# Kernel tuning notes

Measured on AMD Instinct MI355X. Metric: run time of the kernel, lower is better.

The kernel has to match this reference:

```python
import jax, jax.numpy as jnp
import numpy as np

NNZ = 3355443          # int(4096*4096*(1-0.8))
IN_FEATURES = 4096
OUT_FEATURES = 4096
BATCH = 64
ACTIVE_THRESHOLD = 0.01


def setup_inputs() -> dict:
    key = jax.random.key(0)
    k1, k2, k3, k4 = jax.random.split(key, 4)
    x = jax.random.uniform(k1, (BATCH, IN_FEATURES), dtype=jnp.float32)
    row_indices = jax.random.randint(k2, (NNZ,), 0, OUT_FEATURES, dtype=jnp.int32)
    col_indices = jax.random.randint(k3, (NNZ,), 0, IN_FEATURES, dtype=jnp.int32)
    values = jax.random.normal(k4, (NNZ,), dtype=jnp.float32)
    bias = jnp.zeros((OUT_FEATURES,), dtype=jnp.float32)
    return {"x": x, "row_indices": row_indices, "col_indices": col_indices,
            "values": values, "bias": bias}


def reference(x, row_indices, col_indices, values, bias):
    # Event-driven gating: only columns with x > threshold contribute.
    # Equivalent to masking x, then a standard COO spmv per batch row.
    xm = jnp.where(x > ACTIVE_THRESHOLD, x, jnp.zeros((), x.dtype))   # [B, in]
    contrib = values[None, :] * xm[:, col_indices]                    # [B, nnz]
    out = jnp.zeros((x.shape[0], bias.shape[0]), dtype=x.dtype)
    out = out.at[:, row_indices].add(contrib)                         # scatter-add over rows
    return out + bias[None, :]
```

## Files before the change

### kernel.cpp

```cpp
#include <hip/hip_runtime.h>
#include <hip/hip_bf16.h>
#include <stdint.h>

#define IN_F 4096
#define OUT_F 4096
#define NBKT 256
#define SBLOCKS 820
#define REC_PER_SB 4096
#define SMAX 14336u
#define THRESH 0.01f

typedef unsigned int u32;
typedef unsigned short u16;
typedef unsigned char u8;
typedef __attribute__((ext_vector_type(8))) short short8;
typedef __attribute__((ext_vector_type(4))) float f32x4;

static constexpr size_t pad256(size_t x) { return (x + 255u) & ~(size_t)255u; }
static constexpr size_t WS_XB   = 0;
static constexpr size_t WS_CUR  = pad256(WS_XB + (size_t)512 * 64 * 8 * 2);
static constexpr size_t WS_BINS = pad256(WS_CUR + (size_t)NBKT * 4);
static constexpr size_t WS_NEEDED = WS_BINS + (size_t)NBKT * SMAX * 4;

static __device__ __forceinline__ u16 f2bf(float v) {
  __hip_bfloat16 h = __float2bfloat16(v);
  return *reinterpret_cast<u16*>(&h);
}

__global__ __launch_bounds__(256) void k_init(u32* __restrict__ gcursor) {
  gcursor[threadIdx.x] = 0u;
}

__global__ __launch_bounds__(512) void k_scatter(const int* __restrict__ rows,
                                                 const int* __restrict__ cols,
                                                 const float* __restrict__ vals, u32 nnz,
                                                 const float* __restrict__ x,
                                                 u16* __restrict__ xB,
                                                 u32* __restrict__ gcursor,
                                                 u32* __restrict__ sortb) {
  __shared__ u32 cnt[NBKT];
  __shared__ u32 pref[NBKT + 1];
  __shared__ u32 gbase[NBKT];
  __shared__ u32 srt[REC_PER_SB];
  __shared__ u8 srtb[REC_PER_SB];
  const int tid = threadIdx.x;
  const int lane = tid & 63;
  const int wid = tid >> 6;

  if (blockIdx.x < 64) {
    const int g = blockIdx.x * 512 + tid;
    const int b = g & 63;
    const int kg = g >> 6;
    const float* src = x + (size_t)b * IN_F + kg * 8;
    const f32x4 a0 = *reinterpret_cast<const f32x4*>(src);
    const f32x4 a1 = *reinterpret_cast<const f32x4*>(src + 4);
    short8 o;
#pragma unroll
    for (int e = 0; e < 4; ++e) {
      float v = a0[e]; v = (v > THRESH) ? v : 0.0f; o[e] = (short)f2bf(v);
    }
#pragma unroll
    for (int e = 0; e < 4; ++e) {
      float v = a1[e]; v = (v > THRESH) ? v : 0.0f; o[4 + e] = (short)f2bf(v);
    }
    *reinterpret_cast<short8*>(xB + ((size_t)kg * 64 + b) * 8) = o;
  }

  if (tid < NBKT) cnt[tid] = 0;
  __syncthreads();
  const u32 base_i = blockIdx.x * (u32)REC_PER_SB;
  u32 rec[8], bkt[8], rk[8];
#pragma unroll
  for (int j = 0; j < 8; ++j) {
    const u32 i = base_i + (u32)j * 512u + tid;
    bkt[j] = 0xffffffffu;
    if (i < nnz) {
      const u32 r = (u32)rows[i] & 4095u;
      const u32 c = (u32)cols[i] & 4095u;
      rec[j] = (c << 20) | ((r & 15u) << 16) | (u32)f2bf(vals[i]);
      bkt[j] = r >> 4;
      rk[j] = atomicAdd(&cnt[bkt[j]], 1u);
    }
  }
  __syncthreads();
  if (wid == 0) {
    u32 a[4]; u32 s = 0;
#pragma unroll
    for (int j = 0; j < 4; ++j) { a[j] = cnt[lane * 4 + j]; s += a[j]; }
    u32 xx = s;
#pragma unroll
    for (int d = 1; d < 64; d <<= 1) {
      const u32 y = (u32)__shfl_up((int)xx, d, 64);
      if (lane >= d) xx += y;
    }
    u32 e = xx - s;
#pragma unroll
    for (int j = 0; j < 4; ++j) { pref[lane * 4 + j] = e; e += a[j]; }
    if (lane == 63) pref[256] = e;
  }
  __syncthreads();
#pragma unroll
  for (int j = 0; j < 8; ++j)
    if (bkt[j] != 0xffffffffu) {
      const u32 pos = pref[bkt[j]] + rk[j];
      srt[pos] = rec[j];
      srtb[pos] = (u8)bkt[j];
    }
  if (tid < NBKT) {
    const u32 len = pref[tid + 1] - pref[tid];
    gbase[tid] = len ? atomicAdd(&gcursor[tid], len) : 0u;
  }
  __syncthreads();
  const u32 tot = pref[NBKT];
#pragma unroll
  for (int j = 0; j < 8; ++j) {
    const u32 i = (u32)j * 512u + tid;
    if (i < tot) {
      const u32 t = srtb[i];
      const u32 off = gbase[t] + (i - pref[t]);
      if (off < SMAX) sortb[(size_t)t * SMAX + off] = srt[i];
    }
  }
}

__global__ __launch_bounds__(1024, 1) void k_accum(const u32* __restrict__ sortb,
                                                   const u32* __restrict__ ntot,
                                                   const u16* __restrict__ xB,
                                                   const float* __restrict__ bias,
                                                   float* __restrict__ out) {
  __shared__ float W[16 * 1024];
  const int tid = threadIdx.x;
  const int lane = tid & 63;
  const int w = tid >> 6;
  const u32 t = blockIdx.x;
  u32 n = ntot[t];
  if (n > SMAX) n = SMAX;
  const u32* bin = sortb + (size_t)t * SMAX;
  u32 rec[14];
#pragma unroll
  for (int j = 0; j < 14; ++j) {
    const u32 i = (u32)j * 1024u + tid;
    rec[j] = (i < n) ? bin[i] : 0u;
  }

  f32x4 acc0 = {0.f, 0.f, 0.f, 0.f}, acc1 = {0.f, 0.f, 0.f, 0.f};
  f32x4 acc2 = {0.f, 0.f, 0.f, 0.f}, acc3 = {0.f, 0.f, 0.f, 0.f};
  const int row = lane & 15;
  const int e8 = (lane >> 4) * 8;

  for (int q = 0; q < 4; ++q) {
    __syncthreads();
    const f32x4 z = {0.f, 0.f, 0.f, 0.f};
#pragma unroll
    for (int j = 0; j < 4; ++j)
      *reinterpret_cast<f32x4*>(&W[j * 4096 + tid * 4]) = z;
    __syncthreads();
#pragma unroll
    for (int j = 0; j < 14; ++j) {
      const u32 i = (u32)j * 1024u + tid;
      if (i < n) {
        const u32 rc = rec[j];
        if ((rc >> 30) == (u32)q) {
          const u32 rl = (rc >> 16) & 15u;
          const u32 cl = ((rc >> 20) & 1023u) ^ ((rl & 7u) << 3);
          unsafeAtomicAdd(&W[rl * 1024u + cl], __uint_as_float(rc << 16));
        }
      }
    }
    __syncthreads();
#pragma unroll
    for (int s = 0; s < 2; ++s) {
      const int klb = w * 64 + s * 32 + e8;
      const int sw = klb ^ ((row & 7) << 3);
      const f32x4 wa = *reinterpret_cast<const f32x4*>(&W[row * 1024 + sw]);
      const f32x4 wb = *reinterpret_cast<const f32x4*>(&W[row * 1024 + (sw + 4)]);
      short8 af;
#pragma unroll
      for (int e = 0; e < 4; ++e) af[e] = (short)f2bf(wa[e]);
#pragma unroll
      for (int e = 0; e < 4; ++e) af[4 + e] = (short)f2bf(wb[e]);
      const int kabs = q * 1024 + klb;
      const u16* bp = xB + (size_t)(kabs >> 3) * 512 + (u32)row * 8;
      const short8 b0 = *reinterpret_cast<const short8*>(bp);
      const short8 b1 = *reinterpret_cast<const short8*>(bp + 128);
      const short8 b2 = *reinterpret_cast<const short8*>(bp + 256);
      const short8 b3 = *reinterpret_cast<const short8*>(bp + 384);
      acc0 = __builtin_amdgcn_mfma_f32_16x16x32_bf16(af, b0, acc0, 0, 0, 0);
      acc1 = __builtin_amdgcn_mfma_f32_16x16x32_bf16(af, b1, acc1, 0, 0, 0);
      acc2 = __builtin_amdgcn_mfma_f32_16x16x32_bf16(af, b2, acc2, 0, 0, 0);
      acc3 = __builtin_amdgcn_mfma_f32_16x16x32_bf16(af, b3, acc3, 0, 0, 0);
    }
  }
  __syncthreads();
  {
    const int ccol = lane & 15;
    const int rb = (lane >> 4) * 4;
#pragma unroll
    for (int qq = 0; qq < 4; ++qq) W[((w * 4 + 0) * 16 + rb + qq) * 16 + ccol] = acc0[qq];
#pragma unroll
    for (int qq = 0; qq < 4; ++qq) W[((w * 4 + 1) * 16 + rb + qq) * 16 + ccol] = acc1[qq];
#pragma unroll
    for (int qq = 0; qq < 4; ++qq) W[((w * 4 + 2) * 16 + rb + qq) * 16 + ccol] = acc2[qq];
#pragma unroll
    for (int qq = 0; qq < 4; ++qq) W[((w * 4 + 3) * 16 + rb + qq) * 16 + ccol] = acc3[qq];
  }
  __syncthreads();
  const int rl = tid & 15;
  const int b = tid >> 4;
  float sum = bias[t * 16u + rl];
#pragma unroll
  for (int w2 = 0; w2 < 16; ++w2)
    sum += W[((w2 * 4 + (b >> 4)) * 16 + rl) * 16 + (b & 15)];
  out[(size_t)b * OUT_F + t * 16u + rl] = sum;
}

__global__ __launch_bounds__(256) void k_bias_init(const float* __restrict__ bias,
                                                   float* __restrict__ out) {
  const int i = blockIdx.x * 256 + threadIdx.x;
  if (i < 64 * OUT_F) out[i] = bias[i & (OUT_F - 1)];
}

__global__ __launch_bounds__(256) void k_fallback(const int* __restrict__ rows,
                                                  const int* __restrict__ cols,
                                                  const float* __restrict__ vals,
                                                  const float* __restrict__ x,
                                                  float* __restrict__ out, int nnz) {
  const int gw = (int)(((u32)blockIdx.x * blockDim.x + threadIdx.x) >> 6);
  const int lane = threadIdx.x & 63;
  const int nw = (int)(((u32)gridDim.x * blockDim.x) >> 6);
  for (int i = gw; i < nnz; i += nw) {
    const int r = rows[i];
    const int c = cols[i];
    const float v = vals[i];
    const float xv = x[lane * IN_F + c];
    if (xv > THRESH) atomicAdd(&out[(size_t)lane * OUT_F + r], v * xv);
  }
}

extern "C" void kernel_launch(void* const* d_in, const int* in_sizes, int n_in,
                              void* d_out, int out_size, void* d_ws, size_t ws_size,
                              hipStream_t stream) {
  const float* x = (const float*)d_in[0];
  const int* rows = (const int*)d_in[1];
  const int* cols = (const int*)d_in[2];
  const float* vals = (const float*)d_in[3];
  const float* bias = (const float*)d_in[4];
  float* out = (float*)d_out;
  const int nnz = in_sizes[1];

  if (ws_size >= WS_NEEDED && nnz <= SBLOCKS * REC_PER_SB) {
    u16* xB = (u16*)((char*)d_ws + WS_XB);
    u32* gcursor = (u32*)((char*)d_ws + WS_CUR);
    u32* sortb = (u32*)((char*)d_ws + WS_BINS);
    k_init<<<1, 256, 0, stream>>>(gcursor);
    k_scatter<<<SBLOCKS, 512, 0, stream>>>(rows, cols, vals, (u32)nnz, x, xB,
                                           gcursor, sortb);
    k_accum<<<NBKT, 1024, 0, stream>>>(sortb, gcursor, xB, bias, out);
  } else {
    k_bias_init<<<(64 * OUT_F + 255) / 256, 256, 0, stream>>>(bias, out);
    k_fallback<<<4096, 256, 0, stream>>>(rows, cols, vals, x, out, nnz);
  }
}
```

Measured before the change: 65.32 us.

## Fuse init, scatter and accumulate into one cooperative kernel with grid syncs

Replaces the three kernel launches (cursor init, bucket scatter, per-bucket accumulate) with a single cooperative kernel of 256 blocks of 1024 threads, separated by grid-wide barriers and using a shared-memory union for both phases. This removes two launch gaps and the extra pass over gcursor. In exchange the scatter phase now runs on 256 large blocks with about 13K records each instead of 820 smaller blocks, which lowers occupancy and parallelism for that phase. It also adds the cost of cooperative launch and grid syncs.

Result: slower. 120.4 us (+84.3%).

```diff
diff --git a/kernel.cpp b/kernel.cpp
--- a/kernel.cpp
+++ b/kernel.cpp
@@ -1,12 +1,13 @@
 #include <hip/hip_runtime.h>
 #include <hip/hip_bf16.h>
+#include <hip/hip_cooperative_groups.h>
 #include <stdint.h>
 
 #define IN_F 4096
 #define OUT_F 4096
 #define NBKT 256
-#define SBLOCKS 820
-#define REC_PER_SB 4096
+#define NBLK 256
+#define REC_PER_SB 13120
 #define SMAX 14336u
 #define THRESH 0.01f
 
@@ -16,6 +17,8 @@
 typedef __attribute__((ext_vector_type(8))) short short8;
 typedef __attribute__((ext_vector_type(4))) float f32x4;
 
+namespace cg = cooperative_groups;
+
 static constexpr size_t pad256(size_t x) { return (x + 255u) & ~(size_t)255u; }
 static constexpr size_t WS_XB   = 0;
 static constexpr size_t WS_CUR  = pad256(WS_XB + (size_t)512 * 64 * 8 * 2);
@@ -27,28 +30,37 @@
   return *reinterpret_cast<u16*>(&h);
 }
 
-__global__ __launch_bounds__(256) void k_init(u32* __restrict__ gcursor) {
-  gcursor[threadIdx.x] = 0u;
-}
-
-__global__ __launch_bounds__(512) void k_scatter(const int* __restrict__ rows,
-                                                 const int* __restrict__ cols,
-                                                 const float* __restrict__ vals, u32 nnz,
-                                                 const float* __restrict__ x,
-                                                 u16* __restrict__ xB,
-                                                 u32* __restrict__ gcursor,
-                                                 u32* __restrict__ sortb) {
-  __shared__ u32 cnt[NBKT];
-  __shared__ u32 pref[NBKT + 1];
-  __shared__ u32 gbase[NBKT];
-  __shared__ u32 srt[REC_PER_SB];
-  __shared__ u8 srtb[REC_PER_SB];
+struct SmemScatter {
+  u32 cnt[NBKT];
+  u32 pref[NBKT + 1];
+  u32 gbase[NBKT];
+  u32 srt[REC_PER_SB];
+  u8  srtb[REC_PER_SB];
+};
+struct SmemAccum {
+  float W[16 * 1024];
+};
+union Smem { SmemScatter s; SmemAccum a; };
+
+__global__ __launch_bounds__(1024, 1) void k_fused(const int* __restrict__ rows,
+                                                   const int* __restrict__ cols,
+                                                   const float* __restrict__ vals, u32 nnz,
+                                                   const float* __restrict__ x,
+                                                   u16* __restrict__ xB,
+                                                   u32* __restrict__ gcursor,
+                                                   u32* __restrict__ sortb,
+                                                   const float* __restrict__ bias,
+                                                   float* __restrict__ out) {
+  __shared__ Smem sm;
+  cg::grid_group grid = cg::this_grid();
   const int tid = threadIdx.x;
   const int lane = tid & 63;
   const int wid = tid >> 6;
-
-  if (blockIdx.x < 64) {
-    const int g = blockIdx.x * 512 + tid;
+  const u32 blk = blockIdx.x;
+
+  if (tid == 0) gcursor[blk] = 0u;
+  if (tid < 128) {
+    const int g = (int)blk * 128 + tid;
     const int b = g & 63;
     const int kg = g >> 6;
     const float* src = x + (size_t)b * IN_F + kg * 8;
@@ -65,153 +77,149 @@
     }
     *reinterpret_cast<short8*>(xB + ((size_t)kg * 64 + b) * 8) = o;
   }
-
-  if (tid < NBKT) cnt[tid] = 0;
-  __syncthreads();
-  const u32 base_i = blockIdx.x * (u32)REC_PER_SB;
-  u32 rec[8], bkt[8], rk[8];
-#pragma unroll
-  for (int j = 0; j < 8; ++j) {
-    const u32 i = base_i + (u32)j * 512u + tid;
-    bkt[j] = 0xffffffffu;
-    if (i < nnz) {
-      const u32 r = (u32)rows[i] & 4095u;
-      const u32 c = (u32)cols[i] & 4095u;
-      rec[j] = (c << 20) | ((r & 15u) << 16) | (u32)f2bf(vals[i]);
-      bkt[j] = r >> 4;
-      rk[j] = atomicAdd(&cnt[bkt[j]], 1u);
-    }
-  }
-  __syncthreads();
-  if (wid == 0) {
-    u32 a[4]; u32 s = 0;
-#pragma unroll
-    for (int j = 0; j < 4; ++j) { a[j] = cnt[lane * 4 + j]; s += a[j]; }
-    u32 xx = s;
-#pragma unroll
-    for (int d = 1; d < 64; d <<= 1) {
-      const u32 y = (u32)__shfl_up((int)xx, d, 64);
-      if (lane >= d) xx += y;
-    }
-    u32 e = xx - s;
-#pragma unroll
-    for (int j = 0; j < 4; ++j) { pref[lane * 4 + j] = e; e += a[j]; }
-    if (lane == 63) pref[256] = e;
-  }
-  __syncthreads();
-#pragma unroll
-  for (int j = 0; j < 8; ++j)
-    if (bkt[j] != 0xffffffffu) {
-      const u32 pos = pref[bkt[j]] + rk[j];
-      srt[pos] = rec[j];
-      srtb[pos] = (u8)bkt[j];
-    }
-  if (tid < NBKT) {
-    const u32 len = pref[tid + 1] - pref[tid];
-    gbase[tid] = len ? atomicAdd(&gcursor[tid], len) : 0u;
-  }
-  __syncthreads();
-  const u32 tot = pref[NBKT];
-#pragma unroll
-  for (int j = 0; j < 8; ++j) {
-    const u32 i = (u32)j * 512u + tid;
-    if (i < tot) {
-      const u32 t = srtb[i];
-      const u32 off = gbase[t] + (i - pref[t]);
-      if (off < SMAX) sortb[(size_t)t * SMAX + off] = srt[i];
-    }
-  }
-}
-
-__global__ __launch_bounds__(1024, 1) void k_accum(const u32* __restrict__ sortb,
-                                                   const u32* __restrict__ ntot,
-                                                   const u16* __restrict__ xB,
-                                                   const float* __restrict__ bias,
-                                                   float* __restrict__ out) {
-  __shared__ float W[16 * 1024];
-  const int tid = threadIdx.x;
-  const int lane = tid & 63;
-  const int w = tid >> 6;
-  const u32 t = blockIdx.x;
-  u32 n = ntot[t];
-  if (n > SMAX) n = SMAX;
-  const u32* bin = sortb + (size_t)t * SMAX;
-  u32 rec[14];
-#pragma unroll
-  for (int j = 0; j < 14; ++j) {
-    const u32 i = (u32)j * 1024u + tid;
-    rec[j] = (i < n) ? bin[i] : 0u;
-  }
-
-  f32x4 acc0 = {0.f, 0.f, 0.f, 0.f}, acc1 = {0.f, 0.f, 0.f, 0.f};
-  f32x4 acc2 = {0.f, 0.f, 0.f, 0.f}, acc3 = {0.f, 0.f, 0.f, 0.f};
-  const int row = lane & 15;
-  const int e8 = (lane >> 4) * 8;
-
-  for (int q = 0; q < 4; ++q) {
-    __syncthreads();
-    const f32x4 z = {0.f, 0.f, 0.f, 0.f};
-#pragma unroll
-    for (int j = 0; j < 4; ++j)
-      *reinterpret_cast<f32x4*>(&W[j * 4096 + tid * 4]) = z;
-    __syncthreads();
+  if (tid < NBKT) sm.s.cnt[tid] = 0;
+  grid.sync();
+
+  {
+    const u32 base_i = blk * (u32)REC_PER_SB;
+    u32 rec[13], bkt[13], rk[13];
+#pragma unroll
+    for (int j = 0; j < 13; ++j) {
+      const u32 il = (u32)j * 1024u + tid;
+      const u32 i = base_i + il;
+      bkt[j] = 0xffffffffu;
+      if (il < (u32)REC_PER_SB && i < nnz) {
+        const u32 r = (u32)rows[i] & 4095u;
+        const u32 c = (u32)cols[i] & 4095u;
+        rec[j] = (c << 20) | ((r & 15u) << 16) | (u32)f2bf(vals[i]);
+        bkt[j] = r >> 4;
+        rk[j] = atomicAdd(&sm.s.cnt[bkt[j]], 1u);
+      }
+    }
+    __syncthreads();
+    if (wid == 0) {
+      u32 a[4]; u32 s = 0;
+#pragma unroll
+      for (int j = 0; j < 4; ++j) { a[j] = sm.s.cnt[lane * 4 + j]; s += a[j]; }
+      u32 xx = s;
+#pragma unroll
+      for (int d = 1; d < 64; d <<= 1) {
+        const u32 y = (u32)__shfl_up((int)xx, d, 64);
+        if (lane >= d) xx += y;
+      }
+      u32 e = xx - s;
+#pragma unroll
+      for (int j = 0; j < 4; ++j) { sm.s.pref[lane * 4 + j] = e; e += a[j]; }
+      if (lane == 63) sm.s.pref[NBKT] = e;
+    }
+    __syncthreads();
+#pragma unroll
+    for (int j = 0; j < 13; ++j)
+      if (bkt[j] != 0xffffffffu) {
+        const u32 pos = sm.s.pref[bkt[j]] + rk[j];
+        sm.s.srt[pos] = rec[j];
+        sm.s.srtb[pos] = (u8)bkt[j];
+      }
+    if (tid < NBKT) {
+      const u32 len = sm.s.pref[tid + 1] - sm.s.pref[tid];
+      sm.s.gbase[tid] = len ? atomicAdd(&gcursor[tid], len) : 0u;
+    }
+    __syncthreads();
+    const u32 tot = sm.s.pref[NBKT];
+#pragma unroll
+    for (int j = 0; j < 13; ++j) {
+      const u32 i = (u32)j * 1024u + tid;
+      if (i < tot) {
+        const u32 t = sm.s.srtb[i];
+        const u32 off = sm.s.gbase[t] + (i - sm.s.pref[t]);
+        if (off < SMAX) sortb[(size_t)t * SMAX + off] = sm.s.srt[i];
+      }
+    }
+  }
+  grid.sync();
+
+  {
+    const u32 t = blk;
+    u32 n = gcursor[t];
+    if (n > SMAX) n = SMAX;
+    const u32* bin = sortb + (size_t)t * SMAX;
+    u32 rec[14];
 #pragma unroll
     for (int j = 0; j < 14; ++j) {
       const u32 i = (u32)j * 1024u + tid;
-      if (i < n) {
-        const u32 rc = rec[j];
-        if ((rc >> 30) == (u32)q) {
-          const u32 rl = (rc >> 16) & 15u;
-          const u32 cl = ((rc >> 20) & 1023u) ^ ((rl & 7u) << 3);
-          unsafeAtomicAdd(&W[rl * 1024u + cl], __uint_as_float(rc << 16));
+      rec[j] = (i < n) ? bin[i] : 0u;
+    }
+
+    const f32x4 zv = {0.f, 0.f, 0.f, 0.f};
+    f32x4 acc0 = zv, acc1 = zv, acc2 = zv, acc3 = zv;
+    const int row = lane & 15;
+    const int e8 = (lane >> 4) * 8;
+    float* W = sm.a.W;
+
+    for (int q = 0; q < 4; ++q) {
+      __syncthreads();
+#pragma unroll
+      for (int j = 0; j < 4; ++j)
+        *reinterpret_cast<f32x4*>(&W[j * 4096 + tid * 4]) = zv;
+      __syncthreads();
+#pragma unroll
+      for (int j = 0; j < 14; ++j) {
+        const u32 i = (u32)j * 1024u + tid;
+        if (i < n) {
+          const u32 rc = rec[j];
+          if ((rc >> 30) == (u32)q) {
+            const u32 rl = (rc >> 16) & 15u;
+            const u32 cl = ((rc >> 20) & 1023u) ^ ((rl & 7u) << 3);
+            unsafeAtomicAdd(&W[rl * 1024u + cl], __uint_as_float(rc << 16));
+          }
         }
       }
-    }
-    __syncthreads();
-#pragma unroll
-    for (int s = 0; s < 2; ++s) {
-      const int klb = w * 64 + s * 32 + e8;
-      const int sw = klb ^ ((row & 7) << 3);
-      const f32x4 wa = *reinterpret_cast<const f32x4*>(&W[row * 1024 + sw]);
-      const f32x4 wb = *reinterpret_cast<const f32x4*>(&W[row * 1024 + (sw + 4)]);
-      short8 af;
-#pragma unroll
-      for (int e = 0; e < 4; ++e) af[e] = (short)f2bf(wa[e]);
-#pragma unroll
-      for (int e = 0; e < 4; ++e) af[4 + e] = (short)f2bf(wb[e]);
-      const int kabs = q * 1024 + klb;
-      const u16* bp = xB + (size_t)(kabs >> 3) * 512 + (u32)row * 8;
-      const short8 b0 = *reinterpret_cast<const short8*>(bp);
-      const short8 b1 = *reinterpret_cast<const short8*>(bp + 128);
-      const short8 b2 = *reinterpret_cast<const short8*>(bp + 256);
-      const short8 b3 = *reinterpret_cast<const short8*>(bp + 384);
-      acc0 = __builtin_amdgcn_mfma_f32_16x16x32_bf16(af, b0, acc0, 0, 0, 0);
-      acc1 = __builtin_amdgcn_mfma_f32_16x16x32_bf16(af, b1, acc1, 0, 0, 0);
-      acc2 = __builtin_amdgcn_mfma_f32_16x16x32_bf16(af, b2, acc2, 0, 0, 0);
-      acc3 = __builtin_amdgcn_mfma_f32_16x16x32_bf16(af, b3, acc3, 0, 0, 0);
-    }
-  }
-  __syncthreads();
-  {
-    const int ccol = lane & 15;
-    const int rb = (lane >> 4) * 4;
-#pragma unroll
-    for (int qq = 0; qq < 4; ++qq) W[((w * 4 + 0) * 16 + rb + qq) * 16 + ccol] = acc0[qq];
-#pragma unroll
-    for (int qq = 0; qq < 4; ++qq) W[((w * 4 + 1) * 16 + rb + qq) * 16 + ccol] = acc1[qq];
-#pragma unroll
-    for (int qq = 0; qq < 4; ++qq) W[((w * 4 + 2) * 16 + rb + qq) * 16 + ccol] = acc2[qq];
-#pragma unroll
-    for (int qq = 0; qq < 4; ++qq) W[((w * 4 + 3) * 16 + rb + qq) * 16 + ccol] = acc3[qq];
-  }
-  __syncthreads();
-  const int rl = tid & 15;
-  const int b = tid >> 4;
-  float sum = bias[t * 16u + rl];
-#pragma unroll
-  for (int w2 = 0; w2 < 16; ++w2)
-    sum += W[((w2 * 4 + (b >> 4)) * 16 + rl) * 16 + (b & 15)];
-  out[(size_t)b * OUT_F + t * 16u + rl] = sum;
+      __syncthreads();
+#pragma unroll
+      for (int s = 0; s < 2; ++s) {
+        const int klb = wid * 64 + s * 32 + e8;
+        const int sw = klb ^ ((row & 7) << 3);
+        const f32x4 wa = *reinterpret_cast<const f32x4*>(&W[row * 1024 + sw]);
+        const f32x4 wb = *reinterpret_cast<const f32x4*>(&W[row * 1024 + (sw + 4)]);
+        short8 af;
+#pragma unroll
+        for (int e = 0; e < 4; ++e) af[e] = (short)f2bf(wa[e]);
+#pragma unroll
+        for (int e = 0; e < 4; ++e) af[4 + e] = (short)f2bf(wb[e]);
+        const int kabs = q * 1024 + klb;
+        const u16* bp = xB + (size_t)(kabs >> 3) * 512 + (u32)row * 8;
+        const short8 b0 = *reinterpret_cast<const short8*>(bp);
+        const short8 b1 = *reinterpret_cast<const short8*>(bp + 128);
+        const short8 b2 = *reinterpret_cast<const short8*>(bp + 256);
+        const short8 b3 = *reinterpret_cast<const short8*>(bp + 384);
+        acc0 = __builtin_amdgcn_mfma_f32_16x16x32_bf16(af, b0, acc0, 0, 0, 0);
+        acc1 = __builtin_amdgcn_mfma_f32_16x16x32_bf16(af, b1, acc1, 0, 0, 0);
+        acc2 = __builtin_amdgcn_mfma_f32_16x16x32_bf16(af, b2, acc2, 0, 0, 0);
+        acc3 = __builtin_amdgcn_mfma_f32_16x16x32_bf16(af, b3, acc3, 0, 0, 0);
+      }
+    }
+    __syncthreads();
+    {
+      const int ccol = lane & 15;
+      const int rb = (lane >> 4) * 4;
+#pragma unroll
+      for (int qq = 0; qq < 4; ++qq) W[((wid * 4 + 0) * 16 + rb + qq) * 16 + ccol] = acc0[qq];
+#pragma unroll
+      for (int qq = 0; qq < 4; ++qq) W[((wid * 4 + 1) * 16 + rb + qq) * 16 + ccol] = acc1[qq];
+#pragma unroll
+      for (int qq = 0; qq < 4; ++qq) W[((wid * 4 + 2) * 16 + rb + qq) * 16 + ccol] = acc2[qq];
+#pragma unroll
+      for (int qq = 0; qq < 4; ++qq) W[((wid * 4 + 3) * 16 + rb + qq) * 16 + ccol] = acc3[qq];
+    }
+    __syncthreads();
+    const int rl = tid & 15;
+    const int b = tid >> 4;
+    float sum = bias[t * 16u + rl];
+#pragma unroll
+    for (int w2 = 0; w2 < 16; ++w2)
+      sum += W[((w2 * 4 + (b >> 4)) * 16 + rl) * 16 + (b & 15)];
+    out[(size_t)b * OUT_F + t * 16u + rl] = sum;
+  }
 }
 
 __global__ __launch_bounds__(256) void k_bias_init(const float* __restrict__ bias,
@@ -248,14 +256,16 @@
   float* out = (float*)d_out;
   const int nnz = in_sizes[1];
 
-  if (ws_size >= WS_NEEDED && nnz <= SBLOCKS * REC_PER_SB) {
+  if (ws_size >= WS_NEEDED && nnz <= NBLK * REC_PER_SB) {
     u16* xB = (u16*)((char*)d_ws + WS_XB);
     u32* gcursor = (u32*)((char*)d_ws + WS_CUR);
     u32* sortb = (u32*)((char*)d_ws + WS_BINS);
-    k_init<<<1, 256, 0, stream>>>(gcursor);
-    k_scatter<<<SBLOCKS, 512, 0, stream>>>(rows, cols, vals, (u32)nnz, x, xB,
-                                           gcursor, sortb);
-    k_accum<<<NBKT, 1024, 0, stream>>>(sortb, gcursor, xB, bias, out);
+    u32 nnz_u = (u32)nnz;
+    void* args[] = {(void*)&rows, (void*)&cols, (void*)&vals, (void*)&nnz_u,
+                    (void*)&x, (void*)&xB, (void*)&gcursor, (void*)&sortb,
+                    (void*)&bias, (void*)&out};
+    hipLaunchCooperativeKernel((const void*)k_fused, dim3(NBLK), dim3(1024),
+                               args, 0, stream);
   } else {
     k_bias_init<<<(64 * OUT_F + 255) / 256, 256, 0, stream>>>(bias, out);
     k_fallback<<<4096, 256, 0, stream>>>(rows, cols, vals, x, out, nnz);
```
